# Kernel optimization log

Measured on AMD Instinct MI355X. Metric: run time of the kernel, lower is better.

The kernel has to match this reference:

```python
import jax, jax.numpy as jnp
import numpy as np

EPS = 1e-5

def rms_norm(x):
    # SimpleRMSNorm (no learned weight), as used inside BitLinear158
    return x * jax.lax.rsqrt(jnp.mean(x * x, axis=-1, keepdims=True) + EPS)

def act_quant(x):
    # int8 absmax quantization per last-dim row, with straight-through estimator
    scale = 127.0 / jnp.clip(jnp.max(jnp.abs(x), axis=-1, keepdims=True), 1e-5)
    q = jnp.clip(jnp.round(x * scale), -128.0, 127.0) / scale
    return x + jax.lax.stop_gradient(q - x)

def weight_quant(w):
    # ternary {-1,0,1} absmean quantization, with straight-through estimator
    scale = 1.0 / jnp.clip(jnp.mean(jnp.abs(w)), 1e-5)
    q = jnp.clip(jnp.round(w * scale), -1.0, 1.0) / scale
    return w + jax.lax.stop_gradient(q - w)

def bitlinear158(x, w, b):
    xq = act_quant(rms_norm(x))          # [b,s,d_in]
    wq = weight_quant(w)                 # [d_out,d_in]
    return jnp.einsum('bsd,od->bso', xq, wq) + b

def layer_norm(x, g, b):
    mu = jnp.mean(x, axis=-1, keepdims=True)
    var = jnp.mean((x - mu) ** 2, axis=-1, keepdims=True)
    return (x - mu) * jax.lax.rsqrt(var + EPS) * g + b

def setup_inputs() -> dict:
    key = jax.random.key(0)
    ks = jax.random.split(key, 3)
    d, inner = 2048, 8192
    x = jax.random.normal(ks[0], (4, 2048, d), dtype=jnp.float32)
    w1 = jax.random.normal(ks[1], (inner, d), dtype=jnp.float32) * 0.02
    b1 = jnp.zeros((inner,), jnp.float32)
    ln_g = jnp.ones((inner,), jnp.float32)
    ln_b = jnp.zeros((inner,), jnp.float32)
    w2 = jax.random.normal(ks[2], (d, inner), dtype=jnp.float32) * 0.02
    b2 = jnp.zeros((d,), jnp.float32)
    return {"x": x, "w1": w1, "b1": b1, "ln_g": ln_g, "ln_b": ln_b, "w2": w2, "b2": b2}

def reference(x, w1, b1, ln_g, ln_b, w2, b2):
    h = jax.nn.silu(bitlinear158(x, w1, b1))        # project_in: BitLinear158 + SiLU
    h = jax.nn.gelu(h, approximate=False)            # nn.GELU (exact erf form)
    h = layer_norm(h, ln_g, ln_b)                    # nn.LayerNorm(inner_dim)
    return bitlinear158(h, w2, b2)                   # BitLinear158 out projection
```

## Files before the change

kernel.cpp:

```cpp
#include <hip/hip_runtime.h>
#include <hip/hip_bf16.h>
#include <math.h>

typedef __bf16 bf16_t;
typedef __bf16 bf16x4 __attribute__((ext_vector_type(4)));
typedef int i32x4 __attribute__((ext_vector_type(4)));

#define AS1 __attribute__((address_space(1)))
#define AS3 __attribute__((address_space(3)))

__device__ __forceinline__ void gl_lds16(const char* g, char* l) {
  __builtin_amdgcn_global_load_lds((const AS1 void*)g, (AS3 void*)l, 16, 0, 0);
}

__device__ __forceinline__ unsigned pack4i(float a, float b, float c, float d) {
  return ((unsigned)(unsigned char)(int)a) | ((unsigned)(unsigned char)(int)b << 8) |
         ((unsigned)(unsigned char)(int)c << 16) | ((unsigned)(unsigned char)(int)d << 24);
}

__device__ __forceinline__ float block_sum_f(float v) {
  __shared__ float sb[4];
  #pragma unroll
  for (int o = 32; o; o >>= 1) v += __shfl_xor(v, o);
  if ((threadIdx.x & 63) == 0) sb[threadIdx.x >> 6] = v;
  __syncthreads();
  v = sb[0] + sb[1] + sb[2] + sb[3];
  __syncthreads();
  return v;
}
__device__ __forceinline__ float block_max_f(float v) {
  __shared__ float sm[4];
  #pragma unroll
  for (int o = 32; o; o >>= 1) v = fmaxf(v, __shfl_xor(v, o));
  if ((threadIdx.x & 63) == 0) sm[threadIdx.x >> 6] = v;
  __syncthreads();
  v = fmaxf(fmaxf(sm[0], sm[1]), fmaxf(sm[2], sm[3]));
  __syncthreads();
  return v;
}

__global__ __launch_bounds__(256) void wabs_partial(const float* __restrict__ w, int n4,
                                                    double* __restrict__ part) {
  const float4* w4 = (const float4*)w;
  double s = 0.0;
  const int stride = gridDim.x * blockDim.x;
  for (int i = blockIdx.x * blockDim.x + threadIdx.x; i < n4; i += stride) {
    float4 v = w4[i];
    s += (double)fabsf(v.x) + (double)fabsf(v.y) + (double)fabsf(v.z) + (double)fabsf(v.w);
  }
  #pragma unroll
  for (int o = 32; o; o >>= 1) s += __shfl_xor(s, o);
  __shared__ double sd[4];
  if ((threadIdx.x & 63) == 0) sd[threadIdx.x >> 6] = s;
  __syncthreads();
  if (threadIdx.x == 0) part[blockIdx.x] = sd[0] + sd[1] + sd[2] + sd[3];
}

__global__ __launch_bounds__(256) void wabs_final(const double* __restrict__ part, int np,
                                                  double n, float* __restrict__ fwout) {
  double s = 0.0;
  for (int i = threadIdx.x; i < np; i += blockDim.x) s += part[i];
  #pragma unroll
  for (int o = 32; o; o >>= 1) s += __shfl_xor(s, o);
  __shared__ double sd[4];
  if ((threadIdx.x & 63) == 0) sd[threadIdx.x >> 6] = s;
  __syncthreads();
  if (threadIdx.x == 0) {
    double mean = (sd[0] + sd[1] + sd[2] + sd[3]) / n;
    fwout[0] = (float)fmax(mean, 1e-5);
  }
}

__global__ __launch_bounds__(256) void quant_w(const float* __restrict__ w,
                                               const float* __restrict__ fw,
                                               char* __restrict__ wq, int n4) {
  int i = blockIdx.x * blockDim.x + threadIdx.x;
  if (i >= n4) return;
  const float s = 1.0f / fw[0];
  float4 v = ((const float4*)w)[i];
  ((unsigned*)wq)[i] = pack4i(fminf(fmaxf(rintf(v.x * s), -1.f), 1.f),
                              fminf(fmaxf(rintf(v.y * s), -1.f), 1.f),
                              fminf(fmaxf(rintf(v.z * s), -1.f), 1.f),
                              fminf(fmaxf(rintf(v.w * s), -1.f), 1.f));
}

__global__ __launch_bounds__(256) void rms_quant_x(const float* __restrict__ x,
                                                   char* __restrict__ xq,
                                                   float* __restrict__ fx, int K) {
  const int row = blockIdx.x, t = threadIdx.x;
  const size_t base = (size_t)row * K;
  float v[8];
  float ss = 0.f;
  #pragma unroll
  for (int j = 0; j < 2; j++) {
    float4 lv = *(const float4*)(x + base + j * 1024 + t * 4);
    v[j*4+0] = lv.x; v[j*4+1] = lv.y; v[j*4+2] = lv.z; v[j*4+3] = lv.w;
  }
  #pragma unroll
  for (int i = 0; i < 8; i++) ss += v[i] * v[i];
  ss = block_sum_f(ss);
  const float r = 1.0f / sqrtf(ss / (float)K + 1e-5f);
  float amax = 0.f;
  #pragma unroll
  for (int i = 0; i < 8; i++) { v[i] *= r; amax = fmaxf(amax, fabsf(v[i])); }
  amax = block_max_f(amax);
  amax = fmaxf(amax, 1e-5f);
  const float scale = 127.0f / amax;
  #pragma unroll
  for (int j = 0; j < 2; j++) {
    float q[4];
    #pragma unroll
    for (int e = 0; e < 4; e++)
      q[e] = fminf(fmaxf(rintf(v[j*4+e] * scale), -128.f), 127.f);
    *(unsigned*)(xq + base + j * 1024 + t * 4) = pack4i(q[0], q[1], q[2], q[3]);
  }
  if (t == 0) fx[row] = amax / 127.0f;
}

__global__ __launch_bounds__(256) void ln_rms_quant(const bf16_t* __restrict__ h,
                                                    char* __restrict__ hq,
                                                    const float* __restrict__ g,
                                                    const float* __restrict__ bb,
                                                    float* __restrict__ fh, int N) {
  const int row = blockIdx.x, t = threadIdx.x;
  const size_t base = (size_t)row * N;
  float v[32];
  float s = 0.f, ss = 0.f;
  #pragma unroll
  for (int j = 0; j < 8; j++) {
    const int col = j * 1024 + t * 4;
    bf16x4 q = *(const bf16x4*)(h + base + col);
    v[j*4+0] = (float)q[0]; v[j*4+1] = (float)q[1];
    v[j*4+2] = (float)q[2]; v[j*4+3] = (float)q[3];
  }
  #pragma unroll
  for (int i = 0; i < 32; i++) { s += v[i]; ss += v[i] * v[i]; }
  s = block_sum_f(s);
  ss = block_sum_f(ss);
  const float mu = s / (float)N;
  const float var = ss / (float)N - mu * mu;
  const float rstd = 1.0f / sqrtf(var + 1e-5f);
  float ss2 = 0.f;
  #pragma unroll
  for (int j = 0; j < 8; j++) {
    const int col = j * 1024 + t * 4;
    float4 gv = *(const float4*)(g + col);
    float4 bv = *(const float4*)(bb + col);
    float y0 = (v[j*4+0] - mu) * rstd * gv.x + bv.x;
    float y1 = (v[j*4+1] - mu) * rstd * gv.y + bv.y;
    float y2 = (v[j*4+2] - mu) * rstd * gv.z + bv.z;
    float y3 = (v[j*4+3] - mu) * rstd * gv.w + bv.w;
    v[j*4+0] = y0; v[j*4+1] = y1; v[j*4+2] = y2; v[j*4+3] = y3;
    ss2 += y0*y0 + y1*y1 + y2*y2 + y3*y3;
  }
  ss2 = block_sum_f(ss2);
  const float r2 = 1.0f / sqrtf(ss2 / (float)N + 1e-5f);
  float amax = 0.f;
  #pragma unroll
  for (int i = 0; i < 32; i++) { v[i] *= r2; amax = fmaxf(amax, fabsf(v[i])); }
  amax = block_max_f(amax);
  amax = fmaxf(amax, 1e-5f);
  const float scale = 127.0f / amax;
  #pragma unroll
  for (int j = 0; j < 8; j++) {
    const int col = j * 1024 + t * 4;
    float q[4];
    #pragma unroll
    for (int e = 0; e < 4; e++)
      q[e] = fminf(fmaxf(rintf(v[j*4+e] * scale), -128.f), 127.f);
    *(unsigned*)(hq + base + col) = pack4i(q[0], q[1], q[2], q[3]);
  }
  if (t == 0) fh[row] = amax / 127.0f;
}

template<int EPI, bool STORE_BF16>
__global__ __launch_bounds__(512, 2) void gemm256(const char* __restrict__ A,
                                                  const char* __restrict__ B,
                                                  const float* __restrict__ rowf,
                                                  const float* __restrict__ wf,
                                                  const float* __restrict__ bias,
                                                  float* __restrict__ Cf,
                                                  bf16_t* __restrict__ Cb,
                                                  int M, int N, int K) {
  __shared__ char smem[65536];

  const int ntile = N >> 8;
  const int cpx = gridDim.x >> 3;
  const int bid = blockIdx.x;
  const int wg = (bid & 7) * cpx + (bid >> 3);
  const int bm = wg / ntile, bn = wg % ntile;
  const int tm = bm << 8, tn = bn << 8;

  const int tid = threadIdx.x;
  const int w = tid >> 6, lane = tid & 63;
  const int wm = w >> 2, wn = w & 3;
  const int ln15 = lane & 15;

  const int srcRow = lane >> 2;
  const int srcCol = (((lane & 3) ^ ((lane >> 3) & 3)) << 4);
  const size_t KS = (size_t)K;
  const char* pAb = A + (size_t)(tm + w * 16 + srcRow) * KS + srcCol;
  const char* pBb = B + (size_t)(tn + w * 16 + srcRow) * KS + srcCol;
  const size_t hiO = (size_t)128 * KS;
  const int dA = w * 1024;

  const int foff = ln15 * 64 + ((((lane >> 4) ^ ((ln15 >> 1) & 3))) << 4);

  i32x4 acc[8][4] = {};
  const int NT = K >> 6;

#define SB __builtin_amdgcn_sched_barrier(0)
#define BAR { SB; __builtin_amdgcn_s_barrier(); SB; }
#define ST_ALO(bb, kt) gl_lds16(pAb + (size_t)(kt) * 64, smem + (bb) * 16384 + dA);
#define ST_AHI(bb, kt) gl_lds16(pAb + hiO + (size_t)(kt) * 64, smem + (bb) * 16384 + 8192 + dA);
#define ST_BLO(bb, kt) gl_lds16(pBb + (size_t)(kt) * 64, smem + 32768 + (bb) * 16384 + dA);
#define ST_BHI(bb, kt) gl_lds16(pBb + hiO + (size_t)(kt) * 64, smem + 32768 + (bb) * 16384 + 8192 + dA);
#define MM(AF, BF, MB, NB)                                                   \
  _Pragma("unroll") for (int m4 = 0; m4 < 4; m4++)                           \
    _Pragma("unroll") for (int n2 = 0; n2 < 2; n2++)                         \
      acc[(MB)+m4][(NB)+n2] = __builtin_amdgcn_mfma_i32_16x16x64_i8(         \
          AF[m4], BF[n2], acc[(MB)+m4][(NB)+n2], 0, 0, 0);

  ST_ALO(0, 0); ST_AHI(0, 0); ST_BLO(0, 0); ST_BHI(0, 0);
  ST_ALO(1, 1); ST_AHI(1, 1); ST_BLO(1, 1); ST_BHI(1, 1);
  asm volatile("s_waitcnt vmcnt(4)" ::: "memory");
  BAR;

  for (int t = 0; t < NT; ++t) {
    const int b = t & 1;
    const char* sA = smem + b * 16384;
    const char* sB = smem + 32768 + b * 16384;
    i32x4 afL[4], afH[4], bL[2], bH[2];
    #pragma unroll
    for (int m4 = 0; m4 < 4; m4++)
      afL[m4] = *(const i32x4*)(sA + (wm * 4 + m4) * 1024 + foff);
    #pragma unroll
    for (int n2 = 0; n2 < 2; n2++)
      bL[n2] = *(const i32x4*)(sB + (wn * 2 + n2) * 1024 + foff);
    #pragma unroll
    for (int m4 = 0; m4 < 4; m4++)
      afH[m4] = *(const i32x4*)(sA + 8192 + (wm * 4 + m4) * 1024 + foff);
    #pragma unroll
    for (int n2 = 0; n2 < 2; n2++)
      bH[n2] = *(const i32x4*)(sB + 8192 + (wn * 2 + n2) * 1024 + foff);
    __builtin_amdgcn_s_setprio(1);
    MM(afL, bL, 0, 0);
    MM(afH, bL, 4, 0);
    MM(afH, bH, 4, 2);
    MM(afL, bH, 0, 2);
    __builtin_amdgcn_s_setprio(0);
    BAR;
    if (t + 2 < NT) {
      ST_ALO(b, t + 2); ST_AHI(b, t + 2); ST_BLO(b, t + 2); ST_BHI(b, t + 2);
      asm volatile("s_waitcnt vmcnt(4)" ::: "memory");
    } else if (t + 1 < NT) {
      asm volatile("s_waitcnt vmcnt(0)" ::: "memory");
    }
    BAR;
  }
#undef ST_ALO
#undef ST_AHI
#undef ST_BLO
#undef ST_BHI
#undef MM

  const float fwv = wf[0];
  const int rq = (lane >> 4) << 2;
  float rsc[8][4];
  #pragma unroll
  for (int m = 0; m < 8; m++)
    #pragma unroll
    for (int r = 0; r < 4; r++)
      rsc[m][r] = rowf[tm + (m >> 2) * 128 + wm * 64 + (m & 3) * 16 + rq + r] * fwv;

  #pragma unroll
  for (int m = 0; m < 8; m++) {
    #pragma unroll
    for (int n = 0; n < 4; n++) {
      const int col = tn + (n >> 1) * 128 + wn * 32 + (n & 1) * 16 + ln15;
      const float bv = bias[col];
      #pragma unroll
      for (int r = 0; r < 4; r++) {
        const int row = tm + (m >> 2) * 128 + wm * 64 + (m & 3) * 16 + rq + r;
        float val = (float)acc[m][n][r] * rsc[m][r] + bv;
        if (EPI == 1) {
          float sl = val / (1.0f + expf(-val));
          val = 0.5f * sl * (1.0f + erff(sl * 0.70710678118654752f));
        }
        if (STORE_BF16) Cb[(size_t)row * N + col] = (bf16_t)val;
        else            Cf[(size_t)row * N + col] = val;
      }
    }
  }
}

extern "C" void kernel_launch(void* const* d_in, const int* in_sizes, int n_in,
                              void* d_out, int out_size, void* d_ws, size_t ws_size,
                              hipStream_t stream) {
  const float* x   = (const float*)d_in[0];
  const float* w1  = (const float*)d_in[1];
  const float* b1  = (const float*)d_in[2];
  const float* lng = (const float*)d_in[3];
  const float* lnb = (const float*)d_in[4];
  const float* w2  = (const float*)d_in[5];
  const float* b2  = (const float*)d_in[6];
  float* out = (float*)d_out;

  const int inner = in_sizes[2];
  const int d     = in_sizes[1] / inner;
  const int M     = in_sizes[0] / d;

  char* ws = (char*)d_ws;
  size_t off = 0;
  double* part = (double*)(ws + off); off += 1024 * 8;
  float*  fw   = (float*)(ws + off);  off += 256;
  float*  fx   = (float*)(ws + off);  off += (size_t)M * 4;
  float*  fh   = (float*)(ws + off);  off += (size_t)M * 4;
  char*   w1q  = ws + off;            off += (size_t)inner * d;
  char*   w2q  = ws + off;            off += (size_t)inner * d;

  int MC = M;
  while (MC > 256 && off + (size_t)MC * ((size_t)d + 3 * (size_t)inner) > ws_size) MC >>= 1;
  char*   xq = ws + off;              off += (size_t)MC * d;
  bf16_t* h  = (bf16_t*)(ws + off);   off += (size_t)MC * inner * 2;
  char*   hq = ws + off;

  const int nw = inner * d;
  const int n4 = nw / 4;

  wabs_partial<<<1024, 256, 0, stream>>>(w1, n4, part);
  wabs_final<<<1, 256, 0, stream>>>(part, 1024, (double)nw, fw + 0);
  wabs_partial<<<1024, 256, 0, stream>>>(w2, n4, part);
  wabs_final<<<1, 256, 0, stream>>>(part, 1024, (double)nw, fw + 1);
  quant_w<<<n4 / 256, 256, 0, stream>>>(w1, fw + 0, w1q, n4);
  quant_w<<<n4 / 256, 256, 0, stream>>>(w2, fw + 1, w2q, n4);

  for (int mc = 0; mc < M; mc += MC) {
    rms_quant_x<<<MC, 256, 0, stream>>>(x + (size_t)mc * d, xq, fx, d);

    const int g1 = (MC / 256) * (inner / 256);
    gemm256<1, true><<<g1, 512, 0, stream>>>(xq, w1q, fx, fw + 0, b1,
                                             nullptr, h, MC, inner, d);

    ln_rms_quant<<<MC, 256, 0, stream>>>(h, hq, lng, lnb, fh, inner);

    const int g2 = (MC / 256) * (d / 256);
    gemm256<0, false><<<g2, 512, 0, stream>>>(hq, w2q, fh, fw + 1, b2,
                                              out + (size_t)mc * d, nullptr, MC, d, inner);
  }
}
```

Measured before the change: 489.3 us.

## Deepen int8 GEMM pipeline to a 4-stage LDS ring and remap tiles per XCD

The GEMM's shared-memory staging grows from a double buffer to a 4-slot ring of 32KB stages. Loads are now issued three K-tiles ahead, and the loop uses one barrier per iteration instead of two, with graded vmcnt waits near the tail. The block-to-tile mapping also changes: each XCD is given contiguous row bands and iterates over columns, to improve L2 reuse of A rows. Doubling LDS to 128KB per block likely allows only one block per CU despite launch_bounds(512,2), trading occupancy for deeper prefetch.

```diff
diff --git a/kernel.cpp b/kernel.cpp
--- a/kernel.cpp
+++ b/kernel.cpp
@@ -182,12 +182,20 @@
                                                   float* __restrict__ Cf,
                                                   bf16_t* __restrict__ Cb,
                                                   int M, int N, int K) {
-  __shared__ char smem[65536];
+  __shared__ char smem[131072];
 
   const int ntile = N >> 8;
   const int cpx = gridDim.x >> 3;
   const int bid = blockIdx.x;
-  const int wg = (bid & 7) * cpx + (bid >> 3);
+  const int xcd = bid & 7, local = bid >> 3;
+  int wg;
+  const int mrows = cpx / ntile;
+  if (mrows * ntile == cpx && mrows > 0) {
+    const int bm_l = local % mrows, bn_i = local / mrows;
+    wg = (xcd * mrows + bm_l) * ntile + bn_i;
+  } else {
+    wg = xcd * cpx + local;
+  }
   const int bm = wg / ntile, bn = wg % ntile;
   const int tm = bm << 8, tn = bn << 8;
 
@@ -211,25 +219,29 @@
 
 #define SB __builtin_amdgcn_sched_barrier(0)
 #define BAR { SB; __builtin_amdgcn_s_barrier(); SB; }
-#define ST_ALO(bb, kt) gl_lds16(pAb + (size_t)(kt) * 64, smem + (bb) * 16384 + dA);
-#define ST_AHI(bb, kt) gl_lds16(pAb + hiO + (size_t)(kt) * 64, smem + (bb) * 16384 + 8192 + dA);
-#define ST_BLO(bb, kt) gl_lds16(pBb + (size_t)(kt) * 64, smem + 32768 + (bb) * 16384 + dA);
-#define ST_BHI(bb, kt) gl_lds16(pBb + hiO + (size_t)(kt) * 64, smem + 32768 + (bb) * 16384 + 8192 + dA);
+#define ST_ALL(bb, kt) { const size_t ko = (size_t)(kt) * 64;              \
+    gl_lds16(pAb + ko,       smem + ((bb) << 15) + dA);                    \
+    gl_lds16(pAb + hiO + ko, smem + ((bb) << 15) + 8192 + dA);             \
+    gl_lds16(pBb + ko,       smem + ((bb) << 15) + 16384 + dA);            \
+    gl_lds16(pBb + hiO + ko, smem + ((bb) << 15) + 16384 + 8192 + dA); }
 #define MM(AF, BF, MB, NB)                                                   \
   _Pragma("unroll") for (int m4 = 0; m4 < 4; m4++)                           \
     _Pragma("unroll") for (int n2 = 0; n2 < 2; n2++)                         \
       acc[(MB)+m4][(NB)+n2] = __builtin_amdgcn_mfma_i32_16x16x64_i8(         \
           AF[m4], BF[n2], acc[(MB)+m4][(NB)+n2], 0, 0, 0);
 
-  ST_ALO(0, 0); ST_AHI(0, 0); ST_BLO(0, 0); ST_BHI(0, 0);
-  ST_ALO(1, 1); ST_AHI(1, 1); ST_BLO(1, 1); ST_BHI(1, 1);
-  asm volatile("s_waitcnt vmcnt(4)" ::: "memory");
+  ST_ALL(0, 0); ST_ALL(1, 1); ST_ALL(2, 2);
+  asm volatile("s_waitcnt vmcnt(8)" ::: "memory");
   BAR;
 
+  int cur = 0;
   for (int t = 0; t < NT; ++t) {
-    const int b = t & 1;
-    const char* sA = smem + b * 16384;
-    const char* sB = smem + 32768 + b * 16384;
+    const int cb = cur << 15;
+    const int stg = (cur + 3) & 3;
+    if (t + 3 < NT) ST_ALL(stg, t + 3);
+    SB;
+    const char* sA = smem + cb;
+    const char* sB = smem + cb + 16384;
     i32x4 afL[4], afH[4], bL[2], bH[2];
     #pragma unroll
     for (int m4 = 0; m4 < 4; m4++)
@@ -249,19 +261,15 @@
     MM(afH, bH, 4, 2);
     MM(afL, bH, 0, 2);
     __builtin_amdgcn_s_setprio(0);
-    BAR;
-    if (t + 2 < NT) {
-      ST_ALO(b, t + 2); ST_AHI(b, t + 2); ST_BLO(b, t + 2); ST_BHI(b, t + 2);
-      asm volatile("s_waitcnt vmcnt(4)" ::: "memory");
-    } else if (t + 1 < NT) {
-      asm volatile("s_waitcnt vmcnt(0)" ::: "memory");
+    if (t + 1 < NT) {
+      if (t + 3 < NT)      asm volatile("s_waitcnt vmcnt(8)" ::: "memory");
+      else if (t + 2 < NT) asm volatile("s_waitcnt vmcnt(4)" ::: "memory");
+      else                 asm volatile("s_waitcnt vmcnt(0)" ::: "memory");
+      BAR;
     }
-    BAR;
-  }
-#undef ST_ALO
-#undef ST_AHI
-#undef ST_BLO
-#undef ST_BHI
+    cur = (cur + 1) & 3;
+  }
+#undef ST_ALL
 #undef MM
 
   const float fwv = wf[0];
```

Measured after the change: 468.0 us. 4.3% less time.
